# Optimization experiments

Hardware: AMD Instinct MI355X
Metric: run time of the kernel (lower is better)

## Reference

```python
import jax, jax.numpy as jnp
import numpy as np

B, C, H, T, K = 8, 256, 256, 4096, 2  # batch, input_size, hidden_size, seq_len, kernel_size


def setup_inputs() -> dict:
    key = jax.random.key(0)
    ks = jax.random.split(key, 9)
    x = jax.random.normal(ks[0], (B, C, T), dtype=jnp.float32)
    w = lambda k: jax.random.normal(k, (H, C, K), dtype=jnp.float32) * 0.05
    b = lambda k: jax.random.normal(k, (H,), dtype=jnp.float32) * 0.05
    return {
        "x": x,
        "Wz": w(ks[1]), "bz": b(ks[2]),
        "Wf": w(ks[3]), "bf": b(ks[4]),
        "Wo": w(ks[5]), "bo": b(ks[6]),
        "Wi": w(ks[7]), "bi": b(ks[8]),
    }


def _causal_conv(x, W, b):
    # x: [B, C, T], W: [H, C, K]; left-pad by K-1 zeros == torch.cat([zeros, x]) then valid conv
    k = W.shape[-1]
    y = jax.lax.conv_general_dilated(
        x, W, window_strides=(1,), padding=[(k - 1, 0)],
        dimension_numbers=("NCH", "OIH", "NCH"))
    return y + b[None, :, None]


def reference(x, Wz, bz, Wf, bf, Wo, bo, Wi, bi):
    z = jnp.tanh(_causal_conv(x, Wz, bz))          # [B, H, T]
    f = jax.nn.sigmoid(_causal_conv(x, Wf, bf))    # zoneout=0 -> plain sigmoid
    o = jax.nn.sigmoid(_causal_conv(x, Wo, bo))
    i = jax.nn.sigmoid(_causal_conv(x, Wi, bi))    # computed as in original; unused for 'fo' pooling
    del i

    # fo-pooling recurrence: c_t = f_t * c_{t-1} + (1 - f_t) * z_t ; h_t = o_t * c_t
    f_tbh = jnp.transpose(f, (2, 0, 1))  # [T, B, H]
    z_tbh = jnp.transpose(z, (2, 0, 1))
    c0 = jnp.zeros((x.shape[0], Wz.shape[0]), dtype=x.dtype)

    def step(c_prev, fz):
        f_t, z_t = fz
        c_t = f_t * c_prev + (1.0 - f_t) * z_t
        return c_t, c_t

    _, cs = jax.lax.scan(step, c0, (f_tbh, z_tbh))  # [T, B, H]
    c = jnp.transpose(cs, (1, 2, 0))                # [B, H, T]
    h = o * c
    return (h, c)
```

## Files before the change

### kernel.cpp

```cpp
#include <hip/hip_runtime.h>


typedef unsigned short ushort_t;
typedef __attribute__((ext_vector_type(8))) short short8_t;
typedef __attribute__((ext_vector_type(4))) float f32x4;

#define B_ 8
#define C_ 256
#define H_ 256
#define T_ 4096
#define TCH 32
#define NCH 128
#define LZP 129

__device__ __forceinline__ unsigned short f2bf(float f) {
  unsigned int u = __float_as_uint(f);
  u += 0x7fffu + ((u >> 16) & 1u);
  return (unsigned short)(u >> 16);
}
__device__ __forceinline__ float bf2f(unsigned short u) {
  return __uint_as_float(((unsigned int)u) << 16);
}
__device__ __forceinline__ float sigm(float v) { return 1.f / (1.f + __expf(-v)); }
__device__ __forceinline__ float tanh_f(float v) { return 2.f / (1.f + __expf(-2.f * v)) - 1.f; }

__device__ __forceinline__ void gl16(const ushort_t* g, ushort_t* l) {
  __builtin_amdgcn_global_load_lds(
      (const __attribute__((address_space(1))) unsigned int*)g,
      (__attribute__((address_space(3))) unsigned int*)l, 16, 0, 0);
}

__global__ __launch_bounds__(256) void qrnn_pack_x(const float* __restrict__ x,
                                                   ushort_t* __restrict__ xq) {
  __shared__ float tile[32][132];
  const int tid = threadIdx.x;
  const int t0 = blockIdx.x * 128, c0 = blockIdx.y * 32, b = blockIdx.z;
#pragma unroll
  for (int p = 0; p < 5; ++p) {
    const int idx = tid + p * 256;
    if (idx < 1056) {
      const int row = idx / 33, q = idx % 33;
      const int tg = t0 - 4 + q * 4;
      float4 v = make_float4(0.f, 0.f, 0.f, 0.f);
      if (tg >= 0)
        v = *reinterpret_cast<const float4*>(x + ((size_t)(b * C_ + c0 + row)) * T_ + tg);
      tile[row][q * 4 + 0] = v.x; tile[row][q * 4 + 1] = v.y;
      tile[row][q * 4 + 2] = v.z; tile[row][q * 4 + 3] = v.w;
    }
  }
  __syncthreads();
  const int ks0 = c0 >> 5;
#pragma unroll
  for (int q2 = 0; q2 < 2; ++q2) {
    const int p = tid + q2 * 256;
    const int tfl = p >> 6, lane = p & 63;
    const int l15 = lane & 15, g8 = (lane >> 4) * 8;
    const int tcol = tfl * 16 + l15;
    ushort_t o0[8], o1[8];
#pragma unroll
    for (int j = 0; j < 8; ++j) {
      o0[j] = f2bf(tile[g8 + j][tcol + 4]);
      o1[j] = f2bf(tile[g8 + j][tcol + 3]);
    }
    const int tf = (t0 >> 4) + tfl;
    ushort_t* d0 = xq + ((size_t)((b * 256 + tf) * 16 + ks0) * 64 + lane) * 8;
    ushort_t* d1 = xq + ((size_t)((b * 256 + tf) * 16 + 8 + ks0) * 64 + lane) * 8;
    *reinterpret_cast<uint4*>(d0) = *reinterpret_cast<uint4*>(&o0[0]);
    *reinterpret_cast<uint4*>(d1) = *reinterpret_cast<uint4*>(&o1[0]);
  }
}

__global__ __launch_bounds__(256) void qrnn_pack_w(const float* __restrict__ Wz,
                                                   const float* __restrict__ Wf,
                                                   const float* __restrict__ Wo,
                                                   ushort_t* __restrict__ aq) {
  const int idx = blockIdx.x * 256 + threadIdx.x;
  const int lane = idx & 63;
  const int ks = (idx >> 6) & 15;
  const int mf = idx >> 10;
  const int hs = mf / 12, rem = mf % 12;
  const int g = rem >> 2, hlf = rem & 3;
  const int h = hs * 64 + hlf * 16 + (lane & 15);
  const float* W = (g == 0) ? Wz : ((g == 1) ? Wf : Wo);
  ushort_t o[8];
#pragma unroll
  for (int j = 0; j < 8; ++j) {
    const int k = ks * 32 + (lane >> 4) * 8 + j;
    const int c = k & 255;
    const int tap = (k < 256) ? 1 : 0;
    o[j] = f2bf(W[((size_t)h * C_ + c) * 2 + tap]);
  }
  *reinterpret_cast<uint4*>(aq + (size_t)idx * 8) = *reinterpret_cast<uint4*>(&o[0]);
}

__global__ __launch_bounds__(512, 4) void qrnn_g(const ushort_t* __restrict__ aq,
                                                 const ushort_t* __restrict__ xq,
                                                 const float* __restrict__ bz,
                                                 const float* __restrict__ bfv,
                                                 const float* __restrict__ bo,
                                                 float* __restrict__ cl,
                                                 ushort_t* __restrict__ pb,
                                                 ushort_t* __restrict__ ob,
                                                 float* __restrict__ aggP,
                                                 float* __restrict__ aggC) {
  __shared__ __align__(16) char ldsu[66048];
  ushort_t* As = (ushort_t*)ldsu;
  ushort_t* Bs = (ushort_t*)(ldsu + 24576);
  float* lz = (float*)ldsu;
  float* lf = (float*)(ldsu + 33024);

  const int tid = threadIdx.x;
  const int lane = tid & 63;
  const int wid = tid >> 6;
  const int wm = wid >> 1, wt = wid & 1;
  const int l15 = lane & 15, g4 = lane >> 4;
  const int bid = blockIdx.x;
  const int b = bid & 7;
  const int hs = (bid >> 3) & 3;
  const int tt = bid >> 5;

  f32x4 acc[3][4];
#pragma unroll
  for (int i = 0; i < 3; ++i)
#pragma unroll
    for (int n = 0; n < 4; ++n) acc[i][n] = (f32x4){0.f, 0.f, 0.f, 0.f};

  for (int kk = 0; kk < 8; ++kk) {
#pragma unroll
    for (int q = 0; q < 3; ++q) {
      const int c = tid + q * 512;
      gl16(aq + ((size_t)((hs * 12 + (c >> 7)) * 16 + kk * 2 + ((c >> 6) & 1)) << 9) + lane * 8,
           As + (size_t)(c - lane) * 8);
    }
#pragma unroll
    for (int q = 0; q < 2; ++q) {
      const int c2 = tid + q * 512;
      gl16(xq + ((size_t)((b * 256 + tt * 8 + (c2 >> 7)) * 16 + kk * 2 + ((c2 >> 6) & 1)) << 9) +
               lane * 8,
           Bs + (size_t)(c2 - lane) * 8);
    }
    __syncthreads();
#pragma unroll
    for (int l = 0; l < 2; ++l) {
      short8_t a[3], bb[4];
#pragma unroll
      for (int i = 0; i < 3; ++i)
        a[i] = *reinterpret_cast<const short8_t*>(
            &As[(size_t)((((wm * 3 + i) * 2 + l) * 64) + lane) * 8]);
#pragma unroll
      for (int n = 0; n < 4; ++n)
        bb[n] = *reinterpret_cast<const short8_t*>(
            &Bs[(size_t)((((wt * 4 + n) * 2 + l) * 64) + lane) * 8]);
#pragma unroll
      for (int i = 0; i < 3; ++i)
#pragma unroll
        for (int n = 0; n < 4; ++n)
          acc[i][n] = __builtin_amdgcn_mfma_f32_16x16x32_bf16(a[i], bb[n], acc[i][n], 0, 0, 0);
    }
    __syncthreads();
  }

#pragma unroll
  for (int i = 0; i < 3; ++i) {
    const int mfl = wm * 3 + i;
    const int g = mfl >> 2;
    const int hl0 = (mfl & 3) * 16;
    const float* bias = (g == 0) ? bz : ((g == 1) ? bfv : bo);
#pragma unroll
    for (int r = 0; r < 4; ++r) {
      const int hl = hl0 + g4 * 4 + r;
      const float bvv = bias[hs * 64 + hl];
#pragma unroll
      for (int n = 0; n < 4; ++n) {
        const int tl = wt * 64 + n * 16 + l15;
        const float v = acc[i][n][r] + bvv;
        if (g == 0)      lz[hl * LZP + tl] = tanh_f(v);
        else if (g == 1) lf[hl * LZP + tl] = sigm(v);
        else ob[((size_t)b * H_ + hs * 64 + hl) * T_ + tt * 128 + tl] = f2bf(sigm(v));
      }
    }
  }
  __syncthreads();

  if (tid < 256) {
    const int h = tid & 63, ch = tid >> 6;
    float* pz = lz + h * LZP + ch * 32;
    float* pf = lf + h * LZP + ch * 32;
    float c = 0.f, p = 1.f;
#pragma unroll
    for (int t = 0; t < TCH; ++t) {
      const float f = pf[t], z = pz[t];
      c = f * (c - z) + z;
      p *= f;
      pz[t] = c;
      pf[t] = p;
    }
    const int chunkg = tt * 4 + ch;
    aggP[((size_t)b * NCH + chunkg) * H_ + hs * 64 + h] = p;
    aggC[((size_t)b * NCH + chunkg) * H_ + hs * 64 + h] = c;
  }
  __syncthreads();

  float* clb = cl + ((size_t)b * H_ + hs * 64) * T_ + tt * 128;
#pragma unroll
  for (int q = 0; q < 4; ++q) {
    const int j = tid + q * 512;
    const int row = j >> 5, col = (j & 31) * 4;
    float4 v = make_float4(lz[row * LZP + col], lz[row * LZP + col + 1],
                           lz[row * LZP + col + 2], lz[row * LZP + col + 3]);
    *reinterpret_cast<float4*>(clb + (size_t)row * T_ + col) = v;
  }
  ushort_t* pbb = pb + ((size_t)b * H_ + hs * 64) * T_ + tt * 128;
#pragma unroll
  for (int q = 0; q < 2; ++q) {
    const int j = tid + q * 512;
    const int row = j >> 4, col = (j & 15) * 8;
    ushort_t o8[8];
#pragma unroll
    for (int k = 0; k < 8; ++k) o8[k] = f2bf(lf[row * LZP + col + k]);
    *reinterpret_cast<uint4*>(pbb + (size_t)row * T_ + col) = *reinterpret_cast<uint4*>(&o8[0]);
  }
}

__global__ __launch_bounds__(256) void qrnn_s2(const float* __restrict__ aggP,
                                               const float* __restrict__ aggC,
                                               float* __restrict__ cin) {
  const int b = blockIdx.x, h = threadIdx.x;
  float carry = 0.f;
  for (int jb = 0; jb < NCH; jb += 8) {
    float P[8], Cv[8];
#pragma unroll
    for (int u = 0; u < 8; ++u) {
      P[u] = aggP[((size_t)b * NCH + jb + u) * H_ + h];
      Cv[u] = aggC[((size_t)b * NCH + jb + u) * H_ + h];
    }
#pragma unroll
    for (int u = 0; u < 8; ++u) {
      cin[((size_t)b * NCH + jb + u) * H_ + h] = carry;
      carry = Cv[u] + P[u] * carry;
    }
  }
}

__global__ __launch_bounds__(256) void qrnn_s3(const float* __restrict__ cl,
                                               const ushort_t* __restrict__ pb,
                                               const ushort_t* __restrict__ ob,
                                               const float* __restrict__ cin,
                                               float* __restrict__ outc,
                                               float* __restrict__ outh) {
  const int n4 = B_ * H_ * T_ / 4;
  for (int i4 = blockIdx.x * 256 + threadIdx.x; i4 < n4; i4 += gridDim.x * 256) {
    const int idx = i4 << 2;
    const int t = idx & (T_ - 1);
    const int bh = idx >> 12;
    const float carry = cin[((size_t)(bh >> 8) * NCH + (t >> 5)) * H_ + (bh & 255)];
    float4 clv = reinterpret_cast<const float4*>(cl)[i4];
    uint2 pv = reinterpret_cast<const uint2*>(pb)[i4];
    uint2 ov = reinterpret_cast<const uint2*>(ob)[i4];
    const float c0 = clv.x + bf2f((ushort_t)(pv.x & 0xffff)) * carry;
    const float c1 = clv.y + bf2f((ushort_t)(pv.x >> 16)) * carry;
    const float c2 = clv.z + bf2f((ushort_t)(pv.y & 0xffff)) * carry;
    const float c3 = clv.w + bf2f((ushort_t)(pv.y >> 16)) * carry;
    float4 cv = make_float4(c0, c1, c2, c3);
    float4 hv = make_float4(bf2f((ushort_t)(ov.x & 0xffff)) * c0,
                            bf2f((ushort_t)(ov.x >> 16)) * c1,
                            bf2f((ushort_t)(ov.y & 0xffff)) * c2,
                            bf2f((ushort_t)(ov.y >> 16)) * c3);
    reinterpret_cast<float4*>(outc)[i4] = cv;
    reinterpret_cast<float4*>(outh)[i4] = hv;
  }
}

extern "C" void kernel_launch(void* const* d_in, const int* in_sizes, int n_in,
                              void* d_out, int out_size, void* d_ws, size_t ws_size,
                              hipStream_t stream) {
  const float* x  = (const float*)d_in[0];
  const float* Wz = (const float*)d_in[1];
  const float* bz = (const float*)d_in[2];
  const float* Wf = (const float*)d_in[3];
  const float* bfv= (const float*)d_in[4];
  const float* Wo = (const float*)d_in[5];
  const float* bo = (const float*)d_in[6];

  float* outh = (float*)d_out;
  float* outc = outh + (size_t)B_ * H_ * T_;

  constexpr size_t XQ_OFF  = 0;
  constexpr size_t AQ_OFF  = 33554432;
  constexpr size_t CL_OFF  = 34340864;
  constexpr size_t PB_OFF  = 67895296;
  constexpr size_t OB_OFF  = 84672512;
  constexpr size_t AGP_OFF = 101449728;
  constexpr size_t AGC_OFF = 102498304;
  constexpr size_t CIN_OFF = 103546880;
  constexpr size_t WS_NEED = 104595456;
  if (ws_size < WS_NEED) return;

  ushort_t* xq = (ushort_t*)((char*)d_ws + XQ_OFF);
  ushort_t* aq = (ushort_t*)((char*)d_ws + AQ_OFF);
  float* clb   = (float*)((char*)d_ws + CL_OFF);
  ushort_t* pbb= (ushort_t*)((char*)d_ws + PB_OFF);
  ushort_t* ob = (ushort_t*)((char*)d_ws + OB_OFF);
  float* aggP  = (float*)((char*)d_ws + AGP_OFF);
  float* aggC  = (float*)((char*)d_ws + AGC_OFF);
  float* cin   = (float*)((char*)d_ws + CIN_OFF);

  qrnn_pack_x<<<dim3(T_ / 128, C_ / 32, B_), 256, 0, stream>>>(x, xq);
  qrnn_pack_w<<<dim3(192), 256, 0, stream>>>(Wz, Wf, Wo, aq);
  qrnn_g<<<dim3(1024), 512, 0, stream>>>(aq, xq, bz, bfv, bo, clb, pbb, ob, aggP, aggC);
  qrnn_s2<<<dim3(B_), 256, 0, stream>>>(aggP, aggC, cin);
  qrnn_s3<<<dim3(2048), 256, 0, stream>>>(clb, pbb, ob, cin, outc, outh);
}
```

Baseline: 100.1 us.

## Pack x once and build the shifted conv tap at GEMM load time

```diff
diff --git a/kernel.cpp b/kernel.cpp
--- a/kernel.cpp
+++ b/kernel.cpp
@@ -12,6 +12,7 @@
 #define TCH 32
 #define NCH 128
 #define LZP 129
+#define NTF 257
 
 __device__ __forceinline__ unsigned short f2bf(float f) {
   unsigned int u = __float_as_uint(f);
@@ -32,41 +33,34 @@
 
 __global__ __launch_bounds__(256) void qrnn_pack_x(const float* __restrict__ x,
                                                    ushort_t* __restrict__ xq) {
-  __shared__ float tile[32][132];
+  __shared__ float tile[32][129];
   const int tid = threadIdx.x;
   const int t0 = blockIdx.x * 128, c0 = blockIdx.y * 32, b = blockIdx.z;
 #pragma unroll
-  for (int p = 0; p < 5; ++p) {
-    const int idx = tid + p * 256;
-    if (idx < 1056) {
-      const int row = idx / 33, q = idx % 33;
-      const int tg = t0 - 4 + q * 4;
-      float4 v = make_float4(0.f, 0.f, 0.f, 0.f);
-      if (tg >= 0)
-        v = *reinterpret_cast<const float4*>(x + ((size_t)(b * C_ + c0 + row)) * T_ + tg);
-      tile[row][q * 4 + 0] = v.x; tile[row][q * 4 + 1] = v.y;
-      tile[row][q * 4 + 2] = v.z; tile[row][q * 4 + 3] = v.w;
-    }
+  for (int p = 0; p < 4; ++p) {
+    const int j = tid + p * 256;
+    const int row = j >> 5, q = j & 31;
+    float4 v = *reinterpret_cast<const float4*>(x + ((size_t)(b * C_ + c0 + row)) * T_ + t0 + q * 4);
+    tile[row][q * 4 + 0] = v.x; tile[row][q * 4 + 1] = v.y;
+    tile[row][q * 4 + 2] = v.z; tile[row][q * 4 + 3] = v.w;
+  }
+  const int ks0 = c0 >> 5;
+  if (blockIdx.x == 0 && tid < 64) {
+    uint4 zz = make_uint4(0, 0, 0, 0);
+    *reinterpret_cast<uint4*>(xq + ((size_t)(b * NTF) * 8 + ks0) * 512 + tid * 8) = zz;
   }
   __syncthreads();
-  const int ks0 = c0 >> 5;
 #pragma unroll
   for (int q2 = 0; q2 < 2; ++q2) {
     const int p = tid + q2 * 256;
     const int tfl = p >> 6, lane = p & 63;
     const int l15 = lane & 15, g8 = (lane >> 4) * 8;
     const int tcol = tfl * 16 + l15;
-    ushort_t o0[8], o1[8];
-#pragma unroll
-    for (int j = 0; j < 8; ++j) {
-      o0[j] = f2bf(tile[g8 + j][tcol + 4]);
-      o1[j] = f2bf(tile[g8 + j][tcol + 3]);
-    }
-    const int tf = (t0 >> 4) + tfl;
-    ushort_t* d0 = xq + ((size_t)((b * 256 + tf) * 16 + ks0) * 64 + lane) * 8;
-    ushort_t* d1 = xq + ((size_t)((b * 256 + tf) * 16 + 8 + ks0) * 64 + lane) * 8;
+    ushort_t o0[8];
+#pragma unroll
+    for (int j = 0; j < 8; ++j) o0[j] = f2bf(tile[g8 + j][tcol]);
+    ushort_t* d0 = xq + ((size_t)(b * NTF + 1 + (t0 >> 4) + tfl) * 8 + ks0) * 512 + lane * 8;
     *reinterpret_cast<uint4*>(d0) = *reinterpret_cast<uint4*>(&o0[0]);
-    *reinterpret_cast<uint4*>(d1) = *reinterpret_cast<uint4*>(&o1[0]);
   }
 }
 
@@ -93,7 +87,7 @@
   *reinterpret_cast<uint4*>(aq + (size_t)idx * 8) = *reinterpret_cast<uint4*>(&o[0]);
 }
 
-__global__ __launch_bounds__(512, 4) void qrnn_g(const ushort_t* __restrict__ aq,
+__global__ __launch_bounds__(256, 2) void qrnn_g(const ushort_t* __restrict__ aq,
                                                  const ushort_t* __restrict__ xq,
                                                  const float* __restrict__ bz,
                                                  const float* __restrict__ bfv,
@@ -103,56 +97,64 @@
                                                  ushort_t* __restrict__ ob,
                                                  float* __restrict__ aggP,
                                                  float* __restrict__ aggC) {
-  __shared__ __align__(16) char ldsu[66048];
+  __shared__ __align__(16) char ldsu[81920];
   ushort_t* As = (ushort_t*)ldsu;
-  ushort_t* Bs = (ushort_t*)(ldsu + 24576);
+  ushort_t* Bs = (ushort_t*)(ldsu + 49152);
   float* lz = (float*)ldsu;
   float* lf = (float*)(ldsu + 33024);
 
   const int tid = threadIdx.x;
   const int lane = tid & 63;
-  const int wid = tid >> 6;
-  const int wm = wid >> 1, wt = wid & 1;
+  const int w = tid >> 6;
+  const int wm = w >> 1, wt = w & 1;
   const int l15 = lane & 15, g4 = lane >> 4;
   const int bid = blockIdx.x;
   const int b = bid & 7;
   const int hs = (bid >> 3) & 3;
   const int tt = bid >> 5;
 
-  f32x4 acc[3][4];
-#pragma unroll
-  for (int i = 0; i < 3; ++i)
+  const int sh0 = (l15 == 0) ? 1 : 0;
+  const int lane0 = lane + (sh0 ? 15 : -1);
+
+  f32x4 acc[6][4];
+#pragma unroll
+  for (int i = 0; i < 6; ++i)
 #pragma unroll
     for (int n = 0; n < 4; ++n) acc[i][n] = (f32x4){0.f, 0.f, 0.f, 0.f};
 
-  for (int kk = 0; kk < 8; ++kk) {
-#pragma unroll
-    for (int q = 0; q < 3; ++q) {
-      const int c = tid + q * 512;
-      gl16(aq + ((size_t)((hs * 12 + (c >> 7)) * 16 + kk * 2 + ((c >> 6) & 1)) << 9) + lane * 8,
-           As + (size_t)(c - lane) * 8);
-    }
-#pragma unroll
-    for (int q = 0; q < 2; ++q) {
-      const int c2 = tid + q * 512;
-      gl16(xq + ((size_t)((b * 256 + tt * 8 + (c2 >> 7)) * 16 + kk * 2 + ((c2 >> 6) & 1)) << 9) +
-               lane * 8,
-           Bs + (size_t)(c2 - lane) * 8);
+  for (int p = 0; p < 4; ++p) {
+#pragma unroll
+    for (int rr = 0; rr < 20; ++rr) {
+      const int row = w * 20 + rr;
+      if (row < 48) {
+        const int mfl = row >> 2, ksl = row & 3;
+        const int kg = p * 4 + ksl;
+        gl16(aq + (((size_t)(hs * 12 + mfl) * 16 + kg) << 9) + lane * 8, As + row * 512);
+      } else {
+        const int rb = row - 48;
+        const int tfl = rb >> 2, ksl = rb & 3;
+        const int kg = p * 4 + ksl;
+        if (kg < 8) {
+          gl16(xq + (((size_t)(b * NTF + 1 + tt * 8 + tfl) * 8 + kg) << 9) + lane * 8,
+               Bs + rb * 512);
+        } else {
+          gl16(xq + (((size_t)(b * NTF + 1 + tt * 8 + tfl - sh0) * 8 + (kg - 8)) << 9) + lane0 * 8,
+               Bs + rb * 512);
+        }
+      }
     }
     __syncthreads();
 #pragma unroll
-    for (int l = 0; l < 2; ++l) {
-      short8_t a[3], bb[4];
-#pragma unroll
-      for (int i = 0; i < 3; ++i)
-        a[i] = *reinterpret_cast<const short8_t*>(
-            &As[(size_t)((((wm * 3 + i) * 2 + l) * 64) + lane) * 8]);
+    for (int l = 0; l < 4; ++l) {
+      short8_t a[6], bb[4];
+#pragma unroll
+      for (int i = 0; i < 6; ++i)
+        a[i] = *reinterpret_cast<const short8_t*>(&As[(size_t)(((wm * 6 + i) * 4 + l) * 64 + lane) * 8]);
 #pragma unroll
       for (int n = 0; n < 4; ++n)
-        bb[n] = *reinterpret_cast<const short8_t*>(
-            &Bs[(size_t)((((wt * 4 + n) * 2 + l) * 64) + lane) * 8]);
-#pragma unroll
-      for (int i = 0; i < 3; ++i)
+        bb[n] = *reinterpret_cast<const short8_t*>(&Bs[(size_t)(((wt * 4 + n) * 4 + l) * 64 + lane) * 8]);
+#pragma unroll
+      for (int i = 0; i < 6; ++i)
 #pragma unroll
         for (int n = 0; n < 4; ++n)
           acc[i][n] = __builtin_amdgcn_mfma_f32_16x16x32_bf16(a[i], bb[n], acc[i][n], 0, 0, 0);
@@ -161,8 +163,8 @@
   }
 
 #pragma unroll
-  for (int i = 0; i < 3; ++i) {
-    const int mfl = wm * 3 + i;
+  for (int i = 0; i < 6; ++i) {
+    const int mfl = wm * 6 + i;
     const int g = mfl >> 2;
     const int hl0 = (mfl & 3) * 16;
     const float* bias = (g == 0) ? bz : ((g == 1) ? bfv : bo);
@@ -172,7 +174,7 @@
       const float bvv = bias[hs * 64 + hl];
 #pragma unroll
       for (int n = 0; n < 4; ++n) {
-        const int tl = wt * 64 + n * 16 + l15;
+        const int tl = (wt * 4 + n) * 16 + l15;
         const float v = acc[i][n][r] + bvv;
         if (g == 0)      lz[hl * LZP + tl] = tanh_f(v);
         else if (g == 1) lf[hl * LZP + tl] = sigm(v);
@@ -182,43 +184,43 @@
   }
   __syncthreads();
 
-  if (tid < 256) {
+  {
     const int h = tid & 63, ch = tid >> 6;
     float* pz = lz + h * LZP + ch * 32;
     float* pf = lf + h * LZP + ch * 32;
-    float c = 0.f, p = 1.f;
+    float c = 0.f, pcp = 1.f;
 #pragma unroll
     for (int t = 0; t < TCH; ++t) {
       const float f = pf[t], z = pz[t];
       c = f * (c - z) + z;
-      p *= f;
+      pcp *= f;
       pz[t] = c;
-      pf[t] = p;
+      pf[t] = pcp;
     }
     const int chunkg = tt * 4 + ch;
-    aggP[((size_t)b * NCH + chunkg) * H_ + hs * 64 + h] = p;
+    aggP[((size_t)b * NCH + chunkg) * H_ + hs * 64 + h] = pcp;
     aggC[((size_t)b * NCH + chunkg) * H_ + hs * 64 + h] = c;
   }
   __syncthreads();
 
   float* clb = cl + ((size_t)b * H_ + hs * 64) * T_ + tt * 128;
-#pragma unroll
-  for (int q = 0; q < 4; ++q) {
-    const int j = tid + q * 512;
+  ushort_t* pbb = pb + ((size_t)b * H_ + hs * 64) * T_ + tt * 128;
+#pragma unroll
+  for (int q = 0; q < 8; ++q) {
+    const int j = tid + q * 256;
     const int row = j >> 5, col = (j & 31) * 4;
     float4 v = make_float4(lz[row * LZP + col], lz[row * LZP + col + 1],
                            lz[row * LZP + col + 2], lz[row * LZP + col + 3]);
     *reinterpret_cast<float4*>(clb + (size_t)row * T_ + col) = v;
   }
-  ushort_t* pbb = pb + ((size_t)b * H_ + hs * 64) * T_ + tt * 128;
-#pragma unroll
-  for (int q = 0; q < 2; ++q) {
-    const int j = tid + q * 512;
-    const int row = j >> 4, col = (j & 15) * 8;
-    ushort_t o8[8];
-#pragma unroll
-    for (int k = 0; k < 8; ++k) o8[k] = f2bf(lf[row * LZP + col + k]);
-    *reinterpret_cast<uint4*>(pbb + (size_t)row * T_ + col) = *reinterpret_cast<uint4*>(&o8[0]);
+#pragma unroll
+  for (int q = 0; q < 8; ++q) {
+    const int j = tid + q * 256;
+    const int row = j >> 5, col = (j & 31) * 4;
+    ushort_t o4[4];
+    o4[0] = f2bf(lf[row * LZP + col]);     o4[1] = f2bf(lf[row * LZP + col + 1]);
+    o4[2] = f2bf(lf[row * LZP + col + 2]); o4[3] = f2bf(lf[row * LZP + col + 3]);
+    *reinterpret_cast<uint2*>(pbb + (size_t)row * T_ + col) = *reinterpret_cast<uint2*>(&o4[0]);
   }
 }
 
@@ -286,14 +288,14 @@
   float* outc = outh + (size_t)B_ * H_ * T_;
 
   constexpr size_t XQ_OFF  = 0;
-  constexpr size_t AQ_OFF  = 33554432;
-  constexpr size_t CL_OFF  = 34340864;
-  constexpr size_t PB_OFF  = 67895296;
-  constexpr size_t OB_OFF  = 84672512;
-  constexpr size_t AGP_OFF = 101449728;
-  constexpr size_t AGC_OFF = 102498304;
-  constexpr size_t CIN_OFF = 103546880;
-  constexpr size_t WS_NEED = 104595456;
+  constexpr size_t AQ_OFF  = 16842752;
+  constexpr size_t CL_OFF  = 17629184;
+  constexpr size_t PB_OFF  = 51183616;
+  constexpr size_t OB_OFF  = 67960832;
+  constexpr size_t AGP_OFF = 84738048;
+  constexpr size_t AGC_OFF = 85786624;
+  constexpr size_t CIN_OFF = 86835200;
+  constexpr size_t WS_NEED = 87883776;
   if (ws_size < WS_NEED) return;
 
   ushort_t* xq = (ushort_t*)((char*)d_ws + XQ_OFF);
@@ -307,7 +309,7 @@
 
   qrnn_pack_x<<<dim3(T_ / 128, C_ / 32, B_), 256, 0, stream>>>(x, xq);
   qrnn_pack_w<<<dim3(192), 256, 0, stream>>>(Wz, Wf, Wo, aq);
-  qrnn_g<<<dim3(1024), 512, 0, stream>>>(aq, xq, bz, bfv, bo, clb, pbb, ob, aggP, aggC);
+  qrnn_g<<<dim3(1024), 256, 0, stream>>>(aq, xq, bz, bfv, bo, clb, pbb, ob, aggP, aggC);
   qrnn_s2<<<dim3(B_), 256, 0, stream>>>(aggP, aggC, cin);
   qrnn_s3<<<dim3(2048), 256, 0, stream>>>(clb, pbb, ob, cin, outc, outh);
 }
```

Result: slower. 131.8 us (+31.7%).

## Fuse QRNN scan stages into cooperative GEMM kernel with grid sync

Applied to the files above, without the earlier changes.

```diff
diff --git a/kernel.cpp b/kernel.cpp
--- a/kernel.cpp
+++ b/kernel.cpp
@@ -1,4 +1,5 @@
 #include <hip/hip_runtime.h>
+#include <hip/hip_cooperative_groups.h>
 
 
 typedef unsigned short ushort_t;
@@ -11,7 +12,10 @@
 #define T_ 4096
 #define TCH 32
 #define NCH 128
-#define LZP 129
+#define NTF 257
+#define LST 134
+
+namespace cg = cooperative_groups;
 
 __device__ __forceinline__ unsigned short f2bf(float f) {
   unsigned int u = __float_as_uint(f);
@@ -32,41 +36,34 @@
 
 __global__ __launch_bounds__(256) void qrnn_pack_x(const float* __restrict__ x,
                                                    ushort_t* __restrict__ xq) {
-  __shared__ float tile[32][132];
+  __shared__ float tile[32][129];
   const int tid = threadIdx.x;
   const int t0 = blockIdx.x * 128, c0 = blockIdx.y * 32, b = blockIdx.z;
 #pragma unroll
-  for (int p = 0; p < 5; ++p) {
-    const int idx = tid + p * 256;
-    if (idx < 1056) {
-      const int row = idx / 33, q = idx % 33;
-      const int tg = t0 - 4 + q * 4;
-      float4 v = make_float4(0.f, 0.f, 0.f, 0.f);
-      if (tg >= 0)
-        v = *reinterpret_cast<const float4*>(x + ((size_t)(b * C_ + c0 + row)) * T_ + tg);
-      tile[row][q * 4 + 0] = v.x; tile[row][q * 4 + 1] = v.y;
-      tile[row][q * 4 + 2] = v.z; tile[row][q * 4 + 3] = v.w;
-    }
+  for (int p = 0; p < 4; ++p) {
+    const int j = tid + p * 256;
+    const int row = j >> 5, q = j & 31;
+    float4 v = *reinterpret_cast<const float4*>(x + ((size_t)(b * C_ + c0 + row)) * T_ + t0 + q * 4);
+    tile[row][q * 4 + 0] = v.x; tile[row][q * 4 + 1] = v.y;
+    tile[row][q * 4 + 2] = v.z; tile[row][q * 4 + 3] = v.w;
+  }
+  const int ks0 = c0 >> 5;
+  if (blockIdx.x == 0 && tid < 64) {
+    uint4 zz = make_uint4(0, 0, 0, 0);
+    *reinterpret_cast<uint4*>(xq + ((size_t)(b * NTF) * 8 + ks0) * 512 + tid * 8) = zz;
   }
   __syncthreads();
-  const int ks0 = c0 >> 5;
 #pragma unroll
   for (int q2 = 0; q2 < 2; ++q2) {
     const int p = tid + q2 * 256;
     const int tfl = p >> 6, lane = p & 63;
     const int l15 = lane & 15, g8 = (lane >> 4) * 8;
     const int tcol = tfl * 16 + l15;
-    ushort_t o0[8], o1[8];
-#pragma unroll
-    for (int j = 0; j < 8; ++j) {
-      o0[j] = f2bf(tile[g8 + j][tcol + 4]);
-      o1[j] = f2bf(tile[g8 + j][tcol + 3]);
-    }
-    const int tf = (t0 >> 4) + tfl;
-    ushort_t* d0 = xq + ((size_t)((b * 256 + tf) * 16 + ks0) * 64 + lane) * 8;
-    ushort_t* d1 = xq + ((size_t)((b * 256 + tf) * 16 + 8 + ks0) * 64 + lane) * 8;
+    ushort_t o0[8];
+#pragma unroll
+    for (int j = 0; j < 8; ++j) o0[j] = f2bf(tile[g8 + j][tcol]);
+    ushort_t* d0 = xq + ((size_t)(b * NTF + 1 + (t0 >> 4) + tfl) * 8 + ks0) * 512 + lane * 8;
     *reinterpret_cast<uint4*>(d0) = *reinterpret_cast<uint4*>(&o0[0]);
-    *reinterpret_cast<uint4*>(d1) = *reinterpret_cast<uint4*>(&o1[0]);
   }
 }
 
@@ -93,21 +90,22 @@
   *reinterpret_cast<uint4*>(aq + (size_t)idx * 8) = *reinterpret_cast<uint4*>(&o[0]);
 }
 
-__global__ __launch_bounds__(512, 4) void qrnn_g(const ushort_t* __restrict__ aq,
-                                                 const ushort_t* __restrict__ xq,
-                                                 const float* __restrict__ bz,
-                                                 const float* __restrict__ bfv,
-                                                 const float* __restrict__ bo,
-                                                 float* __restrict__ cl,
-                                                 ushort_t* __restrict__ pb,
-                                                 ushort_t* __restrict__ ob,
-                                                 float* __restrict__ aggP,
-                                                 float* __restrict__ aggC) {
-  __shared__ __align__(16) char ldsu[66048];
+template <int COOP>
+__global__ __launch_bounds__(512, 8) void qrnn_g(
+    const ushort_t* __restrict__ aq, const ushort_t* __restrict__ xq,
+    const float* __restrict__ bz, const float* __restrict__ bfv, const float* __restrict__ bo,
+    float* __restrict__ aggPT, float* __restrict__ aggCT,
+    float* __restrict__ outh, float* __restrict__ outc,
+    ushort_t* __restrict__ cl, ushort_t* __restrict__ pb, ushort_t* __restrict__ ob,
+    float* __restrict__ aggP, float* __restrict__ aggC) {
+  __shared__ __align__(16) char ldsu[40960];
   ushort_t* As = (ushort_t*)ldsu;
   ushort_t* Bs = (ushort_t*)(ldsu + 24576);
-  float* lz = (float*)ldsu;
-  float* lf = (float*)(ldsu + 33024);
+  ushort_t* lz  = (ushort_t*)ldsu;
+  ushort_t* lfm = (ushort_t*)(ldsu + 17152);
+  float* aggLP  = (float*)(ldsu + 34304);
+  float* aggLC  = (float*)(ldsu + 35328);
+  float* carrySh = (float*)(ldsu + 36352);
 
   const int tid = threadIdx.x;
   const int lane = tid & 63;
@@ -119,6 +117,9 @@
   const int hs = (bid >> 3) & 3;
   const int tt = bid >> 5;
 
+  const int sh0 = (l15 == 0) ? 1 : 0;
+  const int lane0 = lane + (sh0 ? 15 : -1);
+
   f32x4 acc[3][4];
 #pragma unroll
   for (int i = 0; i < 3; ++i)
@@ -129,15 +130,20 @@
 #pragma unroll
     for (int q = 0; q < 3; ++q) {
       const int c = tid + q * 512;
-      gl16(aq + ((size_t)((hs * 12 + (c >> 7)) * 16 + kk * 2 + ((c >> 6) & 1)) << 9) + lane * 8,
+      gl16(aq + (((size_t)(hs * 12 + (c >> 7)) * 16 + kk * 2 + ((c >> 6) & 1)) << 9) + lane * 8,
            As + (size_t)(c - lane) * 8);
     }
 #pragma unroll
     for (int q = 0; q < 2; ++q) {
       const int c2 = tid + q * 512;
-      gl16(xq + ((size_t)((b * 256 + tt * 8 + (c2 >> 7)) * 16 + kk * 2 + ((c2 >> 6) & 1)) << 9) +
-               lane * 8,
-           Bs + (size_t)(c2 - lane) * 8);
+      const int tfl = c2 >> 7, ksl = (c2 >> 6) & 1;
+      const int kg = kk * 2 + ksl;
+      const ushort_t* src;
+      if (kg < 8)
+        src = xq + (((size_t)(b * NTF + 1 + tt * 8 + tfl) * 8 + kg) << 9) + lane * 8;
+      else
+        src = xq + (((size_t)(b * NTF + 1 + tt * 8 + tfl - sh0) * 8 + (kg - 8)) << 9) + lane0 * 8;
+      gl16(src, Bs + (size_t)(c2 - lane) * 8);
     }
     __syncthreads();
 #pragma unroll
@@ -145,12 +151,10 @@
       short8_t a[3], bb[4];
 #pragma unroll
       for (int i = 0; i < 3; ++i)
-        a[i] = *reinterpret_cast<const short8_t*>(
-            &As[(size_t)((((wm * 3 + i) * 2 + l) * 64) + lane) * 8]);
+        a[i] = *reinterpret_cast<const short8_t*>(&As[(size_t)(((wm * 3 + i) * 2 + l) * 64 + lane) * 8]);
 #pragma unroll
       for (int n = 0; n < 4; ++n)
-        bb[n] = *reinterpret_cast<const short8_t*>(
-            &Bs[(size_t)((((wt * 4 + n) * 2 + l) * 64) + lane) * 8]);
+        bb[n] = *reinterpret_cast<const short8_t*>(&Bs[(size_t)(((wt * 4 + n) * 2 + l) * 64 + lane) * 8]);
 #pragma unroll
       for (int i = 0; i < 3; ++i)
 #pragma unroll
@@ -174,9 +178,12 @@
       for (int n = 0; n < 4; ++n) {
         const int tl = wt * 64 + n * 16 + l15;
         const float v = acc[i][n][r] + bvv;
-        if (g == 0)      lz[hl * LZP + tl] = tanh_f(v);
-        else if (g == 1) lf[hl * LZP + tl] = sigm(v);
-        else ob[((size_t)b * H_ + hs * 64 + hl) * T_ + tt * 128 + tl] = f2bf(sigm(v));
+        if (g == 0)      lz[hl * LST + tl] = f2bf(tanh_f(v));
+        else if (g == 1) lfm[hl * LST + tl] = f2bf(sigm(v) - 0.5f);
+        else {
+          if constexpr (COOP) acc[i][n][r] = sigm(v);
+          else ob[((size_t)b * H_ + hs * 64 + hl) * T_ + tt * 128 + tl] = f2bf(sigm(v));
+        }
       }
     }
   }
@@ -184,41 +191,144 @@
 
   if (tid < 256) {
     const int h = tid & 63, ch = tid >> 6;
-    float* pz = lz + h * LZP + ch * 32;
-    float* pf = lf + h * LZP + ch * 32;
+    const int base = h * LST + ch * 32;
     float c = 0.f, p = 1.f;
 #pragma unroll
-    for (int t = 0; t < TCH; ++t) {
-      const float f = pf[t], z = pz[t];
-      c = f * (c - z) + z;
-      p *= f;
-      pz[t] = c;
-      pf[t] = p;
-    }
-    const int chunkg = tt * 4 + ch;
-    aggP[((size_t)b * NCH + chunkg) * H_ + hs * 64 + h] = p;
-    aggC[((size_t)b * NCH + chunkg) * H_ + hs * 64 + h] = c;
+    for (int u = 0; u < 16; ++u) {
+      const unsigned vz = *reinterpret_cast<const unsigned*>(&lz[base + 2 * u]);
+      const unsigned vf = *reinterpret_cast<const unsigned*>(&lfm[base + 2 * u]);
+      const float f0 = bf2f((ushort_t)(vf & 0xffff)) + 0.5f;
+      const float z0 = bf2f((ushort_t)(vz & 0xffff));
+      c = f0 * (c - z0) + z0; p *= f0;
+      const float cl0 = c, pl0 = p;
+      const float f1 = bf2f((ushort_t)(vf >> 16)) + 0.5f;
+      const float z1 = bf2f((ushort_t)(vz >> 16));
+      c = f1 * (c - z1) + z1; p *= f1;
+      if constexpr (!COOP) {
+        *reinterpret_cast<unsigned*>(&lz[base + 2 * u]) =
+            (unsigned)f2bf(cl0) | ((unsigned)f2bf(c) << 16);
+        *reinterpret_cast<unsigned*>(&lfm[base + 2 * u]) =
+            (unsigned)f2bf(pl0) | ((unsigned)f2bf(p) << 16);
+      }
+    }
+    if constexpr (COOP) {
+      aggLP[ch * 64 + h] = p;
+      aggLC[ch * 64 + h] = c;
+    } else {
+      aggP[((size_t)b * NCH + tt * 4 + ch) * H_ + hs * 64 + h] = p;
+      aggC[((size_t)b * NCH + tt * 4 + ch) * H_ + hs * 64 + h] = c;
+    }
   }
   __syncthreads();
 
-  float* clb = cl + ((size_t)b * H_ + hs * 64) * T_ + tt * 128;
-#pragma unroll
-  for (int q = 0; q < 4; ++q) {
-    const int j = tid + q * 512;
-    const int row = j >> 5, col = (j & 31) * 4;
-    float4 v = make_float4(lz[row * LZP + col], lz[row * LZP + col + 1],
-                           lz[row * LZP + col + 2], lz[row * LZP + col + 3]);
-    *reinterpret_cast<float4*>(clb + (size_t)row * T_ + col) = v;
-  }
-  ushort_t* pbb = pb + ((size_t)b * H_ + hs * 64) * T_ + tt * 128;
-#pragma unroll
-  for (int q = 0; q < 2; ++q) {
-    const int j = tid + q * 512;
-    const int row = j >> 4, col = (j & 15) * 8;
-    ushort_t o8[8];
-#pragma unroll
-    for (int k = 0; k < 8; ++k) o8[k] = f2bf(lf[row * LZP + col + k]);
-    *reinterpret_cast<uint4*>(pbb + (size_t)row * T_ + col) = *reinterpret_cast<uint4*>(&o8[0]);
+  if constexpr (!COOP) {
+    const size_t gb = ((size_t)b * H_ + hs * 64) * T_ + tt * 128;
+#pragma unroll
+    for (int q = 0; q < 2; ++q) {
+      const int j = tid + q * 512;
+      const int row = j >> 4, col = (j & 15) * 8;
+      const int base = row * LST + col;
+      uint4 pk;
+      pk.x = *reinterpret_cast<const unsigned*>(&lz[base]);
+      pk.y = *reinterpret_cast<const unsigned*>(&lz[base + 2]);
+      pk.z = *reinterpret_cast<const unsigned*>(&lz[base + 4]);
+      pk.w = *reinterpret_cast<const unsigned*>(&lz[base + 6]);
+      *reinterpret_cast<uint4*>(cl + gb + (size_t)row * T_ + col) = pk;
+      pk.x = *reinterpret_cast<const unsigned*>(&lfm[base]);
+      pk.y = *reinterpret_cast<const unsigned*>(&lfm[base + 2]);
+      pk.z = *reinterpret_cast<const unsigned*>(&lfm[base + 4]);
+      pk.w = *reinterpret_cast<const unsigned*>(&lfm[base + 6]);
+      *reinterpret_cast<uint4*>(pb + gb + (size_t)row * T_ + col) = pk;
+    }
+    return;
+  } else {
+    if (tid < 64) {
+      float Pt = aggLP[tid], Ct = aggLC[tid];
+#pragma unroll
+      for (int j = 1; j < 4; ++j) {
+        const float Pn = aggLP[j * 64 + tid], Cn = aggLC[j * 64 + tid];
+        Ct = Cn + Pn * Ct;
+        Pt *= Pn;
+      }
+      aggPT[((size_t)b * 32 + tt) * 256 + hs * 64 + tid] = Pt;
+      aggCT[((size_t)b * 32 + tt) * 256 + hs * 64 + tid] = Ct;
+    }
+    __threadfence();
+    cg::this_grid().sync();
+
+    if (tid < 64) {
+      float carry = 0.f;
+      const int hg = hs * 64 + tid;
+#pragma unroll 4
+      for (int j = 0; j < tt; ++j) {
+        const float P = aggPT[((size_t)b * 32 + j) * 256 + hg];
+        const float Cc = aggCT[((size_t)b * 32 + j) * 256 + hg];
+        carry = Cc + P * carry;
+      }
+      carrySh[tid] = carry;
+    }
+    __syncthreads();
+
+    if (tid < 256) {
+      const int h = tid & 63, ch = tid >> 6;
+      float c = carrySh[h];
+#pragma unroll
+      for (int j = 0; j < 3; ++j)
+        if (j < ch) c = aggLC[j * 64 + h] + aggLP[j * 64 + h] * c;
+      const int base = h * LST + ch * 32;
+#pragma unroll
+      for (int u = 0; u < 16; ++u) {
+        const unsigned vz = *reinterpret_cast<const unsigned*>(&lz[base + 2 * u]);
+        const unsigned vf = *reinterpret_cast<const unsigned*>(&lfm[base + 2 * u]);
+        const float f0 = bf2f((ushort_t)(vf & 0xffff)) + 0.5f;
+        const float z0 = bf2f((ushort_t)(vz & 0xffff));
+        c = f0 * (c - z0) + z0;
+        const unsigned c0 = f2bf(c);
+        const float f1 = bf2f((ushort_t)(vf >> 16)) + 0.5f;
+        const float z1 = bf2f((ushort_t)(vz >> 16));
+        c = f1 * (c - z1) + z1;
+        *reinterpret_cast<unsigned*>(&lz[base + 2 * u]) = c0 | ((unsigned)f2bf(c) << 16);
+      }
+    }
+    __syncthreads();
+
+#pragma unroll
+    for (int i = 0; i < 3; ++i) {
+      const int mfl = wm * 3 + i;
+      if ((mfl >> 2) == 2) {
+        const int hl0 = (mfl & 3) * 16;
+#pragma unroll
+        for (int r = 0; r < 4; ++r) {
+          const int hl = hl0 + g4 * 4 + r;
+#pragma unroll
+          for (int n = 0; n < 4; ++n) {
+            const int tl = wt * 64 + n * 16 + l15;
+            lfm[hl * LST + tl] = f2bf(acc[i][n][r]);
+          }
+        }
+      }
+    }
+    __syncthreads();
+
+    const size_t gb = ((size_t)b * H_ + hs * 64) * T_ + tt * 128;
+#pragma unroll
+    for (int q = 0; q < 4; ++q) {
+      const int j = tid + q * 512;
+      const int row = j >> 5, col = (j & 31) * 4;
+      const int base = row * LST + col;
+      const unsigned vc0 = *reinterpret_cast<const unsigned*>(&lz[base]);
+      const unsigned vc1 = *reinterpret_cast<const unsigned*>(&lz[base + 2]);
+      const unsigned vo0 = *reinterpret_cast<const unsigned*>(&lfm[base]);
+      const unsigned vo1 = *reinterpret_cast<const unsigned*>(&lfm[base + 2]);
+      const float c0 = bf2f((ushort_t)(vc0 & 0xffff)), c1 = bf2f((ushort_t)(vc0 >> 16));
+      const float c2v = bf2f((ushort_t)(vc1 & 0xffff)), c3 = bf2f((ushort_t)(vc1 >> 16));
+      const float o0 = bf2f((ushort_t)(vo0 & 0xffff)), o1 = bf2f((ushort_t)(vo0 >> 16));
+      const float o2 = bf2f((ushort_t)(vo1 & 0xffff)), o3 = bf2f((ushort_t)(vo1 >> 16));
+      *reinterpret_cast<float4*>(outc + gb + (size_t)row * T_ + col) =
+          make_float4(c0, c1, c2v, c3);
+      *reinterpret_cast<float4*>(outh + gb + (size_t)row * T_ + col) =
+          make_float4(o0 * c0, o1 * c1, o2 * c2v, o3 * c3);
+    }
   }
 }
 
@@ -242,7 +352,7 @@
   }
 }
 
-__global__ __launch_bounds__(256) void qrnn_s3(const float* __restrict__ cl,
+__global__ __launch_bounds__(256) void qrnn_s3(const ushort_t* __restrict__ cl,
                                                const ushort_t* __restrict__ pb,
                                                const ushort_t* __restrict__ ob,
                                                const float* __restrict__ cin,
@@ -254,20 +364,17 @@
     const int t = idx & (T_ - 1);
     const int bh = idx >> 12;
     const float carry = cin[((size_t)(bh >> 8) * NCH + (t >> 5)) * H_ + (bh & 255)];
-    float4 clv = reinterpret_cast<const float4*>(cl)[i4];
+    uint2 cv2 = reinterpret_cast<const uint2*>(cl)[i4];
     uint2 pv = reinterpret_cast<const uint2*>(pb)[i4];
     uint2 ov = reinterpret_cast<const uint2*>(ob)[i4];
-    const float c0 = clv.x + bf2f((ushort_t)(pv.x & 0xffff)) * carry;
-    const float c1 = clv.y + bf2f((ushort_t)(pv.x >> 16)) * carry;
-    const float c2 = clv.z + bf2f((ushort_t)(pv.y & 0xffff)) * carry;
-    const float c3 = clv.w + bf2f((ushort_t)(pv.y >> 16)) * carry;
-    float4 cv = make_float4(c0, c1, c2, c3);
-    float4 hv = make_float4(bf2f((ushort_t)(ov.x & 0xffff)) * c0,
-                            bf2f((ushort_t)(ov.x >> 16)) * c1,
-                            bf2f((ushort_t)(ov.y & 0xffff)) * c2,
-                            bf2f((ushort_t)(ov.y >> 16)) * c3);
-    reinterpret_cast<float4*>(outc)[i4] = cv;
-    reinterpret_cast<float4*>(outh)[i4] = hv;
+    const float c0 = bf2f((ushort_t)(cv2.x & 0xffff)) + bf2f((ushort_t)(pv.x & 0xffff)) * carry;
+    const float c1 = bf2f((ushort_t)(cv2.x >> 16)) + bf2f((ushort_t)(pv.x >> 16)) * carry;
+    const float c2 = bf2f((ushort_t)(cv2.y & 0xffff)) + bf2f((ushort_t)(pv.y & 0xffff)) * carry;
+    const float c3 = bf2f((ushort_t)(cv2.y >> 16)) + bf2f((ushort_t)(pv.y >> 16)) * carry;
+    reinterpret_cast<float4*>(outc)[i4] = make_float4(c0, c1, c2, c3);
+    reinterpret_cast<float4*>(outh)[i4] =
+        make_float4(bf2f((ushort_t)(ov.x & 0xffff)) * c0, bf2f((ushort_t)(ov.x >> 16)) * c1,
+                    bf2f((ushort_t)(ov.y & 0xffff)) * c2, bf2f((ushort_t)(ov.y >> 16)) * c3);
   }
 }
 
@@ -285,29 +392,48 @@
   float* outh = (float*)d_out;
   float* outc = outh + (size_t)B_ * H_ * T_;
 
-  constexpr size_t XQ_OFF  = 0;
-  constexpr size_t AQ_OFF  = 33554432;
-  constexpr size_t CL_OFF  = 34340864;
-  constexpr size_t PB_OFF  = 67895296;
-  constexpr size_t OB_OFF  = 84672512;
-  constexpr size_t AGP_OFF = 101449728;
-  constexpr size_t AGC_OFF = 102498304;
-  constexpr size_t CIN_OFF = 103546880;
-  constexpr size_t WS_NEED = 104595456;
+  constexpr size_t XQ_OFF   = 0;
+  constexpr size_t AQ_OFF   = 16842752;
+  constexpr size_t AGPT_OFF = 17629184;
+  constexpr size_t AGCT_OFF = 17891328;
+  constexpr size_t CL_OFF   = 18153472;
+  constexpr size_t PB_OFF   = 34930688;
+  constexpr size_t OB_OFF   = 51707904;
+  constexpr size_t AGP_OFF  = 68485120;
+  constexpr size_t AGC_OFF  = 69533696;
+  constexpr size_t CIN_OFF  = 70582272;
+  constexpr size_t WS_NEED  = 71630848;
   if (ws_size < WS_NEED) return;
 
-  ushort_t* xq = (ushort_t*)((char*)d_ws + XQ_OFF);
-  ushort_t* aq = (ushort_t*)((char*)d_ws + AQ_OFF);
-  float* clb   = (float*)((char*)d_ws + CL_OFF);
-  ushort_t* pbb= (ushort_t*)((char*)d_ws + PB_OFF);
-  ushort_t* ob = (ushort_t*)((char*)d_ws + OB_OFF);
-  float* aggP  = (float*)((char*)d_ws + AGP_OFF);
-  float* aggC  = (float*)((char*)d_ws + AGC_OFF);
-  float* cin   = (float*)((char*)d_ws + CIN_OFF);
+  ushort_t* xq   = (ushort_t*)((char*)d_ws + XQ_OFF);
+  ushort_t* aq   = (ushort_t*)((char*)d_ws + AQ_OFF);
+  float* aggPT   = (float*)((char*)d_ws + AGPT_OFF);
+  float* aggCT   = (float*)((char*)d_ws + AGCT_OFF);
+  ushort_t* clb  = (ushort_t*)((char*)d_ws + CL_OFF);
+  ushort_t* pbb  = (ushort_t*)((char*)d_ws + PB_OFF);
+  ushort_t* ob   = (ushort_t*)((char*)d_ws + OB_OFF);
+  float* aggP    = (float*)((char*)d_ws + AGP_OFF);
+  float* aggC    = (float*)((char*)d_ws + AGC_OFF);
+  float* cin     = (float*)((char*)d_ws + CIN_OFF);
 
   qrnn_pack_x<<<dim3(T_ / 128, C_ / 32, B_), 256, 0, stream>>>(x, xq);
   qrnn_pack_w<<<dim3(192), 256, 0, stream>>>(Wz, Wf, Wo, aq);
-  qrnn_g<<<dim3(1024), 512, 0, stream>>>(aq, xq, bz, bfv, bo, clb, pbb, ob, aggP, aggC);
-  qrnn_s2<<<dim3(B_), 256, 0, stream>>>(aggP, aggC, cin);
-  qrnn_s3<<<dim3(2048), 256, 0, stream>>>(clb, pbb, ob, cin, outc, outh);
-}
+
+  int nb = 0;
+  hipOccupancyMaxActiveBlocksPerMultiprocessor(
+      &nb, reinterpret_cast<const void*>(qrnn_g<1>), 512, 0);
+  if (nb >= 4) {
+    const ushort_t* aq_c = aq; const ushort_t* xq_c = xq;
+    const float* bz_c = bz; const float* bf_c = bfv; const float* bo_c = bo;
+    void* params[] = {(void*)&aq_c, (void*)&xq_c, (void*)&bz_c, (void*)&bf_c, (void*)&bo_c,
+                      (void*)&aggPT, (void*)&aggCT, (void*)&outh, (void*)&outc,
+                      (void*)&clb, (void*)&pbb, (void*)&ob, (void*)&aggP, (void*)&aggC};
+    hipLaunchCooperativeKernel(reinterpret_cast<const void*>(qrnn_g<1>),
+                               dim3(1024), dim3(512), params, 0, stream);
+  } else {
+    qrnn_g<0><<<dim3(1024), 512, 0, stream>>>(aq, xq, bz, bfv, bo, aggPT, aggCT, outh, outc,
+                                              clb, pbb, ob, aggP, aggC);
+    qrnn_s2<<<dim3(B_), 256, 0, stream>>>(aggP, aggC, cin);
+    qrnn_s3<<<dim3(2048), 256, 0, stream>>>(clb, pbb, ob, cin, outc, outh);
+  }
+}
```

Result: slower. 381.2 us (+280.8%).
